# Performance work log

Hardware: AMD Instinct MI355X
Metric: run time of the kernel (lower is better)

## Reference

```python
import jax, jax.numpy as jnp
import numpy as np

TOP_K = 4


def setup_inputs() -> dict:
    key = jax.random.key(0)
    ks = jax.random.split(key, 6)
    B, S, H, I, E = 2, 1024, 1024, 1024, 16
    SD = I * 1  # shared_dim = moe_intermediate_size * n_shared_experts
    s = 0.02
    return {
        "hidden_states": jax.random.normal(ks[0], (B, S, H), jnp.float32),
        "gate_w": jax.random.normal(ks[1], (E, H), jnp.float32) * s,
        "w1": jax.random.normal(ks[2], (E, I, H), jnp.float32) * s,
        "w2": jax.random.normal(ks[3], (E, H, I), jnp.float32) * s,
        "shared_gu": jax.random.normal(ks[4], (2 * SD, H), jnp.float32) * s,
        "shared_down": jax.random.normal(ks[5], (H, SD), jnp.float32) * s,
    }


def reference(hidden_states, gate_w, w1, w2, shared_gu, shared_down):
    orig_shape = hidden_states.shape
    H = orig_shape[-1]
    x = hidden_states.reshape(-1, H)            # [T, H]
    T = x.shape[0]
    E = gate_w.shape[0]

    # --- router: softmax -> top-k -> renormalize ---
    logits = x @ gate_w.T                       # [T, E]
    probs = jax.nn.softmax(logits, axis=-1)
    topv, topi = jax.lax.top_k(probs, TOP_K)    # [T, K]
    topv = topv / jnp.sum(topv, axis=-1, keepdims=True)
    # dense routing-weight matrix [T, E] (zero for unselected experts)
    W = jnp.zeros((T, E), x.dtype).at[jnp.arange(T)[:, None], topi].set(topv)

    # --- routed experts: silu(x @ w1[e].T) @ w2[e].T, weighted ---
    h = jax.nn.silu(jnp.einsum('th,eih->tei', x, w1))      # [T, E, I]
    routed = jnp.einsum('tei,ehi,te->th', h, w2, W)        # [T, H]

    # --- shared expert SwiGLU ---
    gu = x @ shared_gu.T                        # [T, 2*SD]
    gate, up = jnp.split(gu, 2, axis=-1)
    shared = (jax.nn.silu(gate) * up) @ shared_down.T      # [T, H]

    return (routed + shared).reshape(orig_shape)
```

## Files before the change

kernel.cpp:

```cpp
#include <hip/hip_runtime.h>
#include <hip/hip_bf16.h>
#include <math.h>

using bf16 = __hip_bfloat16;

typedef __attribute__((ext_vector_type(4))) float fv4;
typedef __attribute__((ext_vector_type(4))) short sh4;
typedef __attribute__((ext_vector_type(8))) short sh8;
typedef __attribute__((ext_vector_type(4))) float f4acc;

#define T_TOK 2048
#define HD    1024
#define NE    16
#define KD    1024
#define NPAIR 8192

static constexpr size_t OFF_XB   = 0;
static constexpr size_t OFF_GUB  = 4194304;
static constexpr size_t OFF_ACT  = 12582912;
static constexpr size_t OFF_H1   = 16777216;
static constexpr size_t OFF_TOPI = 33554432;
static constexpr size_t OFF_TOPV = 33587200;
static constexpr size_t OFF_PTOK = 33619968;
static constexpr size_t OFF_PWT  = 33652736;
static constexpr size_t OFF_OFFS = 33685504;

__device__ __forceinline__ short f2bf(float f) {
  __hip_bfloat16 h = __float2bfloat16(f);
  union { __hip_bfloat16 b; short s; } u; u.b = h; return u.s;
}
__device__ __forceinline__ float bf2f(short s) {
  union { unsigned u; float f; } c; c.u = ((unsigned)(unsigned short)s) << 16; return c.f;
}
__device__ __forceinline__ void async16(const void* g, void* l) {
  __builtin_amdgcn_global_load_lds(
      (const __attribute__((address_space(1))) void*)g,
      (__attribute__((address_space(3))) void*)l, 16, 0, 0);
}

__global__ __launch_bounds__(256) void cast_x_kernel(const float* __restrict__ x,
                                                     bf16* __restrict__ xb) {
  int i = blockIdx.x * 256 + threadIdx.x;
  fv4 v = *(const fv4*)(x + (size_t)i * 4);
  sh4 o; o[0]=f2bf(v[0]); o[1]=f2bf(v[1]); o[2]=f2bf(v[2]); o[3]=f2bf(v[3]);
  *(sh4*)((short*)xb + (size_t)i * 4) = o;
}

__global__ __launch_bounds__(256) void router_kernel(const float* __restrict__ x,
                                                     const float* __restrict__ gw,
                                                     int* __restrict__ topi,
                                                     float* __restrict__ topv) {
  __shared__ float gsh[NE * HD];
  const int tid = threadIdx.x;
  const int wave = tid >> 6;
  const int lane = tid & 63;
  const int t = blockIdx.x * 4 + wave;

#pragma unroll
  for (int r = 0; r < 16; ++r) {
    int idx = r * 256 + tid;
    ((fv4*)gsh)[idx] = ((const fv4*)gw)[idx];
  }

  const float* xr = x + (size_t)t * HD;
  fv4 xa[4];
#pragma unroll
  for (int q = 0; q < 4; ++q) xa[q] = *(const fv4*)(xr + q * 256 + lane * 4);

  __syncthreads();

  float p[NE];
#pragma unroll
  for (int e = 0; e < NE; ++e) {
    const float* g = gsh + e * HD;
    float a = 0.f;
#pragma unroll
    for (int q = 0; q < 4; ++q) {
      fv4 gv = *(const fv4*)(g + q * 256 + lane * 4);
      a += xa[q][0] * gv[0] + xa[q][1] * gv[1] + xa[q][2] * gv[2] + xa[q][3] * gv[3];
    }
    p[e] = a;
  }
#pragma unroll
  for (int off = 1; off < 64; off <<= 1) {
#pragma unroll
    for (int e = 0; e < NE; ++e) p[e] += __shfl_xor(p[e], off);
  }

  int sel_i[4]; float sel_v[4];
#pragma unroll
  for (int k = 0; k < 4; ++k) {
    float best = p[0]; int bi = 0;
#pragma unroll
    for (int e = 1; e < NE; ++e) {
      bool c = p[e] > best;
      best = c ? p[e] : best;
      bi   = c ? e : bi;
    }
    sel_i[k] = bi; sel_v[k] = best;
#pragma unroll
    for (int e = 0; e < NE; ++e) p[e] = (e == bi) ? -3.4e38f : p[e];
  }
  float m = sel_v[0];
  float e0 = expf(sel_v[0] - m), e1 = expf(sel_v[1] - m);
  float e2 = expf(sel_v[2] - m), e3 = expf(sel_v[3] - m);
  float inv = 1.f / (e0 + e1 + e2 + e3);

  if (lane == 0) {
    topi[t * 4 + 0] = sel_i[0]; topv[t * 4 + 0] = e0 * inv;
    topi[t * 4 + 1] = sel_i[1]; topv[t * 4 + 1] = e1 * inv;
    topi[t * 4 + 2] = sel_i[2]; topv[t * 4 + 2] = e2 * inv;
    topi[t * 4 + 3] = sel_i[3]; topv[t * 4 + 3] = e3 * inv;
  }
}

__global__ __launch_bounds__(1024) void route_build_kernel(const int* __restrict__ topi,
                                                           const float* __restrict__ topv,
                                                           int* __restrict__ offsets,
                                                           int* __restrict__ pair_token,
                                                           float* __restrict__ pair_weight) {
  __shared__ int tsh[NPAIR];
  __shared__ int cnt_sh[NE];
  __shared__ int off_sh[NE + 1];
  const int tid = threadIdx.x;
  const int wave = tid >> 6;
  const int lane = tid & 63;

#pragma unroll
  for (int r = 0; r < NPAIR / 1024; ++r) tsh[r * 1024 + tid] = topi[r * 1024 + tid];
  __syncthreads();

  const int e = wave;
  int cnt = 0;
  for (int c = 0; c < NPAIR; c += 64) {
    unsigned long long msk = __ballot(tsh[c + lane] == e);
    cnt += __popcll(msk);
  }
  if (lane == 0) cnt_sh[e] = cnt;
  __syncthreads();
  if (tid == 0) {
    int acc = 0;
    for (int i = 0; i < NE; ++i) { off_sh[i] = acc; acc += cnt_sh[i]; }
    off_sh[NE] = acc;
  }
  __syncthreads();
  if (tid <= NE) offsets[tid] = off_sh[tid];

  int base = off_sh[e];
  for (int c = 0; c < NPAIR; c += 64) {
    bool match = (tsh[c + lane] == e);
    unsigned long long msk = __ballot(match);
    unsigned long long lt = (lane == 0) ? 0ull : ((~0ull) >> (64 - lane));
    int pre = __popcll(msk & lt);
    if (match) {
      int slot = base + pre;
      pair_token[slot] = (c + lane) >> 2;
      pair_weight[slot] = topv[c + lane];
    }
    base += __popcll(msk);
  }
}

__global__ __launch_bounds__(256) void act_kernel(const short* __restrict__ gub,
                                                  short* __restrict__ act) {
  int i = blockIdx.x * 256 + threadIdx.x;
  int t = i >> 8, g = i & 255;
  sh4 gs = *(const sh4*)(gub + (size_t)t * 2048 + g * 4);
  sh4 us = *(const sh4*)(gub + (size_t)t * 2048 + 1024 + g * 4);
  sh4 o;
#pragma unroll
  for (int q = 0; q < 4; ++q) {
    float gg = bf2f(gs[q]);
    float s = gg / (1.f + expf(-gg)) * bf2f(us[q]);
    o[q] = f2bf(s);
  }
  *(sh4*)(act + (size_t)t * 1024 + g * 4) = o;
}

template <int PHASE>
__global__ __launch_bounds__(256) void gemm_pair_kernel(
    const bf16* __restrict__ A_sh, const bf16* __restrict__ A_rt,
    const float* __restrict__ B_sh, const float* __restrict__ B_rt,
    void* __restrict__ O_sh, void* __restrict__ O_rt,
    const int* __restrict__ ptok, const float* __restrict__ pwt,
    const int* __restrict__ offsets) {
  __shared__ bf16 Ash[3][128][32];
  __shared__ bf16 Bsh[2][128][32];

  const int tid = threadIdx.x;
  const int lane = tid & 63;
  const int wave = tid >> 6;
  const int wm = wave >> 1, wn = wave & 1;

  const bool routed = (int)blockIdx.x < 2048;
  int mt, nt, seg_start = 0, count = 0;
  const bf16* Abase;
  const float* Bpanel;
  if (routed) {
    int bid = blockIdx.x;
    int e = bid & 15;
    int r = bid >> 4;
    mt = r >> 3; nt = r & 7;
    seg_start = offsets[e];
    count = offsets[e + 1] - seg_start;
    if (mt * 128 >= count) return;
    Abase = A_rt;
    Bpanel = B_rt + ((size_t)e << 20) + (size_t)(nt * 128) * KD;
  } else {
    int sb = blockIdx.x - 2048;
    constexpr int nwg = (PHASE == 0) ? 256 : 128;
    constexpr int cpx = nwg >> 3;
    int sw = (sb & 7) * cpx + (sb >> 3);
    nt = sw >> 4; mt = sw & 15;
    count = 1 << 30;
    Abase = A_sh;
    Bpanel = B_sh + (size_t)(nt * 128) * KD;
  }

  const int agsw = ((lane & 3) ^ ((lane >> 3) & 3)) * 8;
  const bf16* arow[2];
#pragma unroll
  for (int r = 0; r < 2; ++r) {
    int rowloc = r * 64 + wave * 16 + (lane >> 2);
    int grow;
    if (routed) {
      int slot = seg_start + mt * 128 + rowloc;
      if (slot > NPAIR - 1) slot = NPAIR - 1;
      grow = (PHASE == 0) ? ptok[slot] : slot;
    } else {
      grow = mt * 128 + rowloc;
    }
    arow[r] = Abase + (size_t)grow * KD + agsw;
  }

  const float* brow[4];
  int bwrow[4], bwcol[4];
#pragma unroll
  for (int r = 0; r < 4; ++r) {
    int idx = (r << 8) + tid;
    int row = idx >> 3, cg = idx & 7;
    brow[r] = Bpanel + (size_t)row * KD + (cg << 2);
    int blkp = (cg >> 1) ^ ((row >> 1) & 3);
    bwrow[r] = row; bwcol[r] = blkp * 8 + (cg & 1) * 4;
  }

  const int rsw = ((lane & 15) >> 1) & 3;
  const int colsw = ((lane >> 4) ^ rsw) * 8;

  f4acc acc[4][4];
#pragma unroll
  for (int i = 0; i < 4; ++i)
#pragma unroll
    for (int j = 0; j < 4; ++j) acc[i][j] = (f4acc)(0.f);

  {
    fv4 b0 = *(const fv4*)(brow[0]);
    fv4 b1 = *(const fv4*)(brow[1]);
    fv4 b2 = *(const fv4*)(brow[2]);
    fv4 b3 = *(const fv4*)(brow[3]);
    async16(arow[0],      (void*)&Ash[0][wave * 16][0]);
    async16(arow[1],      (void*)&Ash[0][64 + wave * 16][0]);
    async16(arow[0] + 32, (void*)&Ash[1][wave * 16][0]);
    async16(arow[1] + 32, (void*)&Ash[1][64 + wave * 16][0]);
    sh4 p0; p0[0]=f2bf(b0[0]); p0[1]=f2bf(b0[1]); p0[2]=f2bf(b0[2]); p0[3]=f2bf(b0[3]);
    sh4 p1; p1[0]=f2bf(b1[0]); p1[1]=f2bf(b1[1]); p1[2]=f2bf(b1[2]); p1[3]=f2bf(b1[3]);
    sh4 p2; p2[0]=f2bf(b2[0]); p2[1]=f2bf(b2[1]); p2[2]=f2bf(b2[2]); p2[3]=f2bf(b2[3]);
    sh4 p3; p3[0]=f2bf(b3[0]); p3[1]=f2bf(b3[1]); p3[2]=f2bf(b3[2]); p3[3]=f2bf(b3[3]);
    *(sh4*)&Bsh[0][bwrow[0]][bwcol[0]] = p0;
    *(sh4*)&Bsh[0][bwrow[1]][bwcol[1]] = p1;
    *(sh4*)&Bsh[0][bwrow[2]][bwcol[2]] = p2;
    *(sh4*)&Bsh[0][bwrow[3]][bwcol[3]] = p3;
    asm volatile("s_waitcnt vmcnt(2)" ::: "memory");
    asm volatile("s_waitcnt lgkmcnt(0)" ::: "memory");
    __builtin_amdgcn_sched_barrier(0);
    __builtin_amdgcn_s_barrier();
  }

  int c3 = 0;
  for (int kt = 0; kt < 32; ++kt) {
    fv4 b0, b1, b2, b3;
    const bool hn = (kt < 31);
    if (hn) {
      const int kn1 = (kt + 1) * 32;
      b0 = *(const fv4*)(brow[0] + kn1);
      b1 = *(const fv4*)(brow[1] + kn1);
      b2 = *(const fv4*)(brow[2] + kn1);
      b3 = *(const fv4*)(brow[3] + kn1);
      if (kt < 30) {
        const int kn2 = (kt + 2) * 32;
        int a2 = c3 + 2; if (a2 >= 3) a2 -= 3;
        async16(arow[0] + kn2, (void*)&Ash[a2][wave * 16][0]);
        async16(arow[1] + kn2, (void*)&Ash[a2][64 + wave * 16][0]);
      }
    }
    __builtin_amdgcn_sched_barrier(0);

    sh8 fa[4], fb[4];
#pragma unroll
    for (int mi = 0; mi < 4; ++mi)
      fa[mi] = *(const sh8*)&Ash[c3][wm * 64 + mi * 16 + (lane & 15)][colsw];
#pragma unroll
    for (int ni = 0; ni < 4; ++ni)
      fb[ni] = *(const sh8*)&Bsh[kt & 1][wn * 64 + ni * 16 + (lane & 15)][colsw];
#pragma unroll
    for (int mi = 0; mi < 4; ++mi)
#pragma unroll
      for (int ni = 0; ni < 4; ++ni)
        acc[mi][ni] = __builtin_amdgcn_mfma_f32_16x16x32_bf16(fa[mi], fb[ni], acc[mi][ni], 0, 0, 0);

    if (hn) {
      if (kt < 30) asm volatile("s_waitcnt vmcnt(2)" ::: "memory");
      else         asm volatile("s_waitcnt vmcnt(0)" ::: "memory");
      __builtin_amdgcn_sched_barrier(0);
      const int nb = (kt + 1) & 1;
      sh4 p0; p0[0]=f2bf(b0[0]); p0[1]=f2bf(b0[1]); p0[2]=f2bf(b0[2]); p0[3]=f2bf(b0[3]);
      sh4 p1; p1[0]=f2bf(b1[0]); p1[1]=f2bf(b1[1]); p1[2]=f2bf(b1[2]); p1[3]=f2bf(b1[3]);
      sh4 p2; p2[0]=f2bf(b2[0]); p2[1]=f2bf(b2[1]); p2[2]=f2bf(b2[2]); p2[3]=f2bf(b2[3]);
      sh4 p3; p3[0]=f2bf(b3[0]); p3[1]=f2bf(b3[1]); p3[2]=f2bf(b3[2]); p3[3]=f2bf(b3[3]);
      *(sh4*)&Bsh[nb][bwrow[0]][bwcol[0]] = p0;
      *(sh4*)&Bsh[nb][bwrow[1]][bwcol[1]] = p1;
      *(sh4*)&Bsh[nb][bwrow[2]][bwcol[2]] = p2;
      *(sh4*)&Bsh[nb][bwrow[3]][bwcol[3]] = p3;
      asm volatile("s_waitcnt lgkmcnt(0)" ::: "memory");
      __builtin_amdgcn_sched_barrier(0);
      __builtin_amdgcn_s_barrier();
    }
    c3 += 1; if (c3 == 3) c3 = 0;
  }

  if (PHASE == 0) {
    if (routed) {
#pragma unroll
      for (int mi = 0; mi < 4; ++mi) {
#pragma unroll
        for (int j = 0; j < 4; ++j) {
          int rloc = wm * 64 + mi * 16 + (lane >> 4) * 4 + j;
          if (mt * 128 + rloc >= count) continue;
          size_t orow = (size_t)(seg_start + mt * 128 + rloc) * 1024 + nt * 128;
#pragma unroll
          for (int ni = 0; ni < 4; ++ni) {
            int cloc = wn * 64 + ni * 16 + (lane & 15);
            float v = acc[mi][ni][j];
            float s = v / (1.f + expf(-v));
            ((short*)O_rt)[orow + cloc] = f2bf(s);
          }
        }
      }
    } else {
#pragma unroll
      for (int mi = 0; mi < 4; ++mi) {
#pragma unroll
        for (int j = 0; j < 4; ++j) {
          int rloc = wm * 64 + mi * 16 + (lane >> 4) * 4 + j;
          size_t orow = (size_t)(mt * 128 + rloc) * 2048 + nt * 128;
#pragma unroll
          for (int ni = 0; ni < 4; ++ni) {
            int cloc = wn * 64 + ni * 16 + (lane & 15);
            ((short*)O_sh)[orow + cloc] = f2bf(acc[mi][ni][j]);
          }
        }
      }
    }
  } else {
    if (routed) {
#pragma unroll
      for (int mi = 0; mi < 4; ++mi) {
#pragma unroll
        for (int j = 0; j < 4; ++j) {
          int rloc = wm * 64 + mi * 16 + (lane >> 4) * 4 + j;
          if (mt * 128 + rloc >= count) continue;
          int slot = seg_start + mt * 128 + rloc;
          int token = ptok[slot];
          float w = pwt[slot];
          float* orow = (float*)O_rt + (size_t)token * 1024 + nt * 128;
#pragma unroll
          for (int ni = 0; ni < 4; ++ni) {
            int cloc = wn * 64 + ni * 16 + (lane & 15);
            unsafeAtomicAdd(orow + cloc, w * acc[mi][ni][j]);
          }
        }
      }
    } else {
#pragma unroll
      for (int mi = 0; mi < 4; ++mi) {
#pragma unroll
        for (int j = 0; j < 4; ++j) {
          int rloc = wm * 64 + mi * 16 + (lane >> 4) * 4 + j;
          float* orow = (float*)O_sh + (size_t)(mt * 128 + rloc) * 1024 + nt * 128;
#pragma unroll
          for (int ni = 0; ni < 4; ++ni) {
            int cloc = wn * 64 + ni * 16 + (lane & 15);
            unsafeAtomicAdd(orow + cloc, acc[mi][ni][j]);
          }
        }
      }
    }
  }
}

extern "C" void kernel_launch(void* const* d_in, const int* in_sizes, int n_in,
                              void* d_out, int out_size, void* d_ws, size_t ws_size,
                              hipStream_t stream) {
  const float* x   = (const float*)d_in[0];
  const float* gw  = (const float*)d_in[1];
  const float* w1  = (const float*)d_in[2];
  const float* w2  = (const float*)d_in[3];
  const float* sgu = (const float*)d_in[4];
  const float* sdn = (const float*)d_in[5];
  float* out = (float*)d_out;

  char* ws = (char*)d_ws;
  bf16*  xb    = (bf16*)(ws + OFF_XB);
  bf16*  gub   = (bf16*)(ws + OFF_GUB);
  bf16*  act   = (bf16*)(ws + OFF_ACT);
  bf16*  h1    = (bf16*)(ws + OFF_H1);
  int*   topi  = (int*)(ws + OFF_TOPI);
  float* topv  = (float*)(ws + OFF_TOPV);
  int*   ptok  = (int*)(ws + OFF_PTOK);
  float* pwt   = (float*)(ws + OFF_PWT);
  int*   offs  = (int*)(ws + OFF_OFFS);

  hipMemsetAsync(d_out, 0, (size_t)out_size * sizeof(float), stream);

  cast_x_kernel<<<2048, 256, 0, stream>>>(x, xb);
  router_kernel<<<512, 256, 0, stream>>>(x, gw, topi, topv);
  route_build_kernel<<<1, 1024, 0, stream>>>(topi, topv, offs, ptok, pwt);

  gemm_pair_kernel<0><<<2304, 256, 0, stream>>>(xb, xb, sgu, w1,
                                                gub, h1, ptok, pwt, offs);
  act_kernel<<<2048, 256, 0, stream>>>((const short*)gub, (short*)act);

  gemm_pair_kernel<1><<<2176, 256, 0, stream>>>(act, h1, sdn, w2,
                                                out, out, ptok, pwt, offs);
}
```

Measured before the change: 190.5 us.

## Deepen GEMM prefetch to two k-tiles and drop LDS swizzling

Raises the fp32 weight register prefetch from one k-tile ahead to two, using ping-pong register sets in a 2x-unrolled loop. The A buffer moves from a 3-stage to a 4-stage LDS ring, indexed by kt&3. The XOR swizzles on LDS writes and reads are removed in favour of plain row-major layout. The aim is to hide global load latency better, at the cost of more registers and possible LDS bank conflicts now that the swizzle is gone.

```diff
diff --git a/kernel.cpp b/kernel.cpp
--- a/kernel.cpp
+++ b/kernel.cpp
@@ -184,7 +184,7 @@
     void* __restrict__ O_sh, void* __restrict__ O_rt,
     const int* __restrict__ ptok, const float* __restrict__ pwt,
     const int* __restrict__ offsets) {
-  __shared__ bf16 Ash[3][128][32];
+  __shared__ bf16 Ash[4][128][32];
   __shared__ bf16 Bsh[2][128][32];
 
   const int tid = threadIdx.x;
@@ -217,7 +217,6 @@
     Bpanel = B_sh + (size_t)(nt * 128) * KD;
   }
 
-  const int agsw = ((lane & 3) ^ ((lane >> 3) & 3)) * 8;
   const bf16* arow[2];
 #pragma unroll
   for (int r = 0; r < 2; ++r) {
@@ -230,7 +229,7 @@
     } else {
       grow = mt * 128 + rowloc;
     }
-    arow[r] = Abase + (size_t)grow * KD + agsw;
+    arow[r] = Abase + (size_t)grow * KD + (lane & 3) * 8;
   }
 
   const float* brow[4];
@@ -240,12 +239,8 @@
     int idx = (r << 8) + tid;
     int row = idx >> 3, cg = idx & 7;
     brow[r] = Bpanel + (size_t)row * KD + (cg << 2);
-    int blkp = (cg >> 1) ^ ((row >> 1) & 3);
-    bwrow[r] = row; bwcol[r] = blkp * 8 + (cg & 1) * 4;
-  }
-
-  const int rsw = ((lane & 15) >> 1) & 3;
-  const int colsw = ((lane >> 4) ^ rsw) * 8;
+    bwrow[r] = row; bwcol[r] = cg << 2;
+  }
 
   f4acc acc[4][4];
 #pragma unroll
@@ -253,79 +248,67 @@
 #pragma unroll
     for (int j = 0; j < 4; ++j) acc[i][j] = (f4acc)(0.f);
 
+  fv4 ra[4], rb[4];
+
   {
-    fv4 b0 = *(const fv4*)(brow[0]);
-    fv4 b1 = *(const fv4*)(brow[1]);
-    fv4 b2 = *(const fv4*)(brow[2]);
-    fv4 b3 = *(const fv4*)(brow[3]);
+#pragma unroll
+    for (int r = 0; r < 4; ++r) ra[r] = *(const fv4*)(brow[r]);
     async16(arow[0],      (void*)&Ash[0][wave * 16][0]);
     async16(arow[1],      (void*)&Ash[0][64 + wave * 16][0]);
     async16(arow[0] + 32, (void*)&Ash[1][wave * 16][0]);
     async16(arow[1] + 32, (void*)&Ash[1][64 + wave * 16][0]);
-    sh4 p0; p0[0]=f2bf(b0[0]); p0[1]=f2bf(b0[1]); p0[2]=f2bf(b0[2]); p0[3]=f2bf(b0[3]);
-    sh4 p1; p1[0]=f2bf(b1[0]); p1[1]=f2bf(b1[1]); p1[2]=f2bf(b1[2]); p1[3]=f2bf(b1[3]);
-    sh4 p2; p2[0]=f2bf(b2[0]); p2[1]=f2bf(b2[1]); p2[2]=f2bf(b2[2]); p2[3]=f2bf(b2[3]);
-    sh4 p3; p3[0]=f2bf(b3[0]); p3[1]=f2bf(b3[1]); p3[2]=f2bf(b3[2]); p3[3]=f2bf(b3[3]);
-    *(sh4*)&Bsh[0][bwrow[0]][bwcol[0]] = p0;
-    *(sh4*)&Bsh[0][bwrow[1]][bwcol[1]] = p1;
-    *(sh4*)&Bsh[0][bwrow[2]][bwcol[2]] = p2;
-    *(sh4*)&Bsh[0][bwrow[3]][bwcol[3]] = p3;
-    asm volatile("s_waitcnt vmcnt(2)" ::: "memory");
+#pragma unroll
+    for (int r = 0; r < 4; ++r) rb[r] = *(const fv4*)(brow[r] + 32);
+#pragma unroll
+    for (int r = 0; r < 4; ++r) {
+      sh4 p; p[0]=f2bf(ra[r][0]); p[1]=f2bf(ra[r][1]); p[2]=f2bf(ra[r][2]); p[3]=f2bf(ra[r][3]);
+      *(sh4*)&Bsh[0][bwrow[r]][bwcol[r]] = p;
+    }
     asm volatile("s_waitcnt lgkmcnt(0)" ::: "memory");
-    __builtin_amdgcn_sched_barrier(0);
+    asm volatile("s_waitcnt vmcnt(6)" ::: "memory");
     __builtin_amdgcn_s_barrier();
   }
 
-  int c3 = 0;
-  for (int kt = 0; kt < 32; ++kt) {
-    fv4 b0, b1, b2, b3;
-    const bool hn = (kt < 31);
-    if (hn) {
-      const int kn1 = (kt + 1) * 32;
-      b0 = *(const fv4*)(brow[0] + kn1);
-      b1 = *(const fv4*)(brow[1] + kn1);
-      b2 = *(const fv4*)(brow[2] + kn1);
-      b3 = *(const fv4*)(brow[3] + kn1);
-      if (kt < 30) {
-        const int kn2 = (kt + 2) * 32;
-        int a2 = c3 + 2; if (a2 >= 3) a2 -= 3;
-        async16(arow[0] + kn2, (void*)&Ash[a2][wave * 16][0]);
-        async16(arow[1] + kn2, (void*)&Ash[a2][64 + wave * 16][0]);
-      }
-    }
-    __builtin_amdgcn_sched_barrier(0);
+  auto body = [&](int kt, fv4 (&src)[4], fv4 (&dst)[4]) {
+    if (kt < 30) {
+      const int k2 = (kt + 2) * 32;
+      const int a2 = (kt + 2) & 3;
+      async16(arow[0] + k2, (void*)&Ash[a2][wave * 16][0]);
+      async16(arow[1] + k2, (void*)&Ash[a2][64 + wave * 16][0]);
+#pragma unroll
+      for (int r = 0; r < 4; ++r) dst[r] = *(const fv4*)(brow[r] + k2);
+    }
 
     sh8 fa[4], fb[4];
 #pragma unroll
     for (int mi = 0; mi < 4; ++mi)
-      fa[mi] = *(const sh8*)&Ash[c3][wm * 64 + mi * 16 + (lane & 15)][colsw];
+      fa[mi] = *(const sh8*)&Ash[kt & 3][wm * 64 + mi * 16 + (lane & 15)][(lane >> 4) * 8];
 #pragma unroll
     for (int ni = 0; ni < 4; ++ni)
-      fb[ni] = *(const sh8*)&Bsh[kt & 1][wn * 64 + ni * 16 + (lane & 15)][colsw];
+      fb[ni] = *(const sh8*)&Bsh[kt & 1][wn * 64 + ni * 16 + (lane & 15)][(lane >> 4) * 8];
 #pragma unroll
     for (int mi = 0; mi < 4; ++mi)
 #pragma unroll
       for (int ni = 0; ni < 4; ++ni)
         acc[mi][ni] = __builtin_amdgcn_mfma_f32_16x16x32_bf16(fa[mi], fb[ni], acc[mi][ni], 0, 0, 0);
 
-    if (hn) {
-      if (kt < 30) asm volatile("s_waitcnt vmcnt(2)" ::: "memory");
+    if (kt < 31) {
+      const int nb = (kt + 1) & 1;
+#pragma unroll
+      for (int r = 0; r < 4; ++r) {
+        sh4 p; p[0]=f2bf(src[r][0]); p[1]=f2bf(src[r][1]); p[2]=f2bf(src[r][2]); p[3]=f2bf(src[r][3]);
+        *(sh4*)&Bsh[nb][bwrow[r]][bwcol[r]] = p;
+      }
+      asm volatile("s_waitcnt lgkmcnt(0)" ::: "memory");
+      if (kt < 30) asm volatile("s_waitcnt vmcnt(6)" ::: "memory");
       else         asm volatile("s_waitcnt vmcnt(0)" ::: "memory");
-      __builtin_amdgcn_sched_barrier(0);
-      const int nb = (kt + 1) & 1;
-      sh4 p0; p0[0]=f2bf(b0[0]); p0[1]=f2bf(b0[1]); p0[2]=f2bf(b0[2]); p0[3]=f2bf(b0[3]);
-      sh4 p1; p1[0]=f2bf(b1[0]); p1[1]=f2bf(b1[1]); p1[2]=f2bf(b1[2]); p1[3]=f2bf(b1[3]);
-      sh4 p2; p2[0]=f2bf(b2[0]); p2[1]=f2bf(b2[1]); p2[2]=f2bf(b2[2]); p2[3]=f2bf(b2[3]);
-      sh4 p3; p3[0]=f2bf(b3[0]); p3[1]=f2bf(b3[1]); p3[2]=f2bf(b3[2]); p3[3]=f2bf(b3[3]);
-      *(sh4*)&Bsh[nb][bwrow[0]][bwcol[0]] = p0;
-      *(sh4*)&Bsh[nb][bwrow[1]][bwcol[1]] = p1;
-      *(sh4*)&Bsh[nb][bwrow[2]][bwcol[2]] = p2;
-      *(sh4*)&Bsh[nb][bwrow[3]][bwcol[3]] = p3;
-      asm volatile("s_waitcnt lgkmcnt(0)" ::: "memory");
-      __builtin_amdgcn_sched_barrier(0);
       __builtin_amdgcn_s_barrier();
     }
-    c3 += 1; if (c3 == 3) c3 = 0;
+  };
+
+  for (int kt = 0; kt < 32; kt += 2) {
+    body(kt, rb, ra);
+    body(kt + 1, ra, rb);
   }
 
   if (PHASE == 0) {
```

Result: slower. 213.4 us (+12.1%).
